# Kernel optimization log

Measured on AMD Instinct MI355X. Metric: run time of the kernel, lower is better.

The kernel has to match this reference:

```python
import jax, jax.numpy as jnp
import numpy as np

N_NODES = 100000
D = 128        # hidden_channels
H = 64         # hidden_size
E = 8192       # num_hyperedges
K = 32         # nodes per hyperedge (fixed group size)


def setup_inputs() -> dict:
    key = jax.random.key(0)
    k1, k2, k3, k4, k5, k6 = jax.random.split(key, 6)
    X = jax.random.normal(k1, (N_NODES, D), dtype=jnp.float32)
    idx = jax.random.randint(k2, (E, K), 0, N_NODES, dtype=jnp.int64)
    # per-hyperedge MLP params (torch Linear: y = x @ W.T + b), scaled like
    # torch's default uniform fan-in init magnitude
    W1 = jax.random.normal(k3, (E, H, D), dtype=jnp.float32) / np.sqrt(D)
    b1 = jax.random.normal(k4, (E, H), dtype=jnp.float32) / np.sqrt(D)
    W2 = jax.random.normal(k5, (E, H), dtype=jnp.float32) / np.sqrt(H)
    b2 = jax.random.normal(k6, (E,), dtype=jnp.float32) / np.sqrt(H)
    return {"X": X, "idx": idx, "W1": W1, "b1": b1, "W2": W2, "b2": b2}


def reference(X, idx, W1, b1, W2, b2):
    # gather node features per hyperedge: [E, K, D]
    x_he = X[idx]
    # per-edge 2-layer MLP scorer (leaky_relu slope 0.01 = torch default)
    h = jax.nn.leaky_relu(jnp.einsum('ekd,ehd->ekh', x_he, W1) + b1[:, None, :])
    w = jnp.einsum('ekh,eh->ek', h, W2) + b2[:, None]          # [E, K]
    beta = jax.nn.softmax(w, axis=1)                           # softmax over group
    z = jnp.einsum('ek,ekd->ed', beta, x_he)                   # weighted sum reduce
    Z = jnp.tanh(jax.nn.leaky_relu(z))                         # [E, D]
    return Z, beta
```

## Files before the change

### kernel.cpp

```cpp
#include <hip/hip_runtime.h>

#define E_EDGES 8192
#define KN 32
#define DD 128
#define HH 64
#define XPAD 8

typedef __attribute__((ext_vector_type(8))) __bf16 bf16x8;
typedef __attribute__((ext_vector_type(8))) unsigned short u16x8;
typedef __attribute__((ext_vector_type(4))) float f32x4;

__device__ __forceinline__ unsigned short f2bf(float f) {
    unsigned int u = __builtin_bit_cast(unsigned int, f);
    u += 0x7FFFu + ((u >> 16) & 1u);
    return (unsigned short)(u >> 16);
}

__device__ __forceinline__ bf16x8 pack_bf8(float4 a, float4 b) {
    u16x8 u;
    u[0] = f2bf(a.x); u[1] = f2bf(a.y); u[2] = f2bf(a.z); u[3] = f2bf(a.w);
    u[4] = f2bf(b.x); u[5] = f2bf(b.y); u[6] = f2bf(b.z); u[7] = f2bf(b.w);
    return __builtin_bit_cast(bf16x8, u);
}

__global__ __launch_bounds__(256, 4)
void he_attn_kernel(const float* __restrict__ X,
                    const int* __restrict__ idx,
                    const float* __restrict__ W1,
                    const float* __restrict__ b1,
                    const float* __restrict__ W2,
                    const float* __restrict__ b2,
                    float* __restrict__ Zout,
                    float* __restrict__ Bout)
{
    const int e    = blockIdx.x;
    const int tid  = threadIdx.x;
    const int lane = tid & 63;
    const int wv   = tid >> 6;
    const int cl   = lane & 15;
    const int kg   = lane >> 4;

    __shared__ unsigned short xsb[KN][DD + XPAD];
    __shared__ float wpart[4][KN];
    __shared__ float beta_s[KN];

    const int j = wv * 16 + cl;
    const float* W1r = W1 + ((size_t)e * HH + j) * DD;
    float4 wf[8];
    #pragma unroll
    for (int kc = 0; kc < 4; ++kc) {
        wf[2 * kc]     = *reinterpret_cast<const float4*>(W1r + kc * 32 + kg * 8);
        wf[2 * kc + 1] = *reinterpret_cast<const float4*>(W1r + kc * 32 + kg * 8 + 4);
    }

    #pragma unroll
    for (int it = 0; it < 4; ++it) {
        int i = tid + it * 256;
        int k = i >> 5;
        int c = i & 31;
        int row = idx[e * KN + k];
        float4 v = reinterpret_cast<const float4*>(X)[(size_t)row * (DD / 4) + c];
        ushort4 bv;
        bv.x = f2bf(v.x); bv.y = f2bf(v.y); bv.z = f2bf(v.z); bv.w = f2bf(v.w);
        *reinterpret_cast<ushort4*>(&xsb[k][c * 4]) = bv;
    }
    __syncthreads();

    f32x4 acc0 = {0.f, 0.f, 0.f, 0.f};
    f32x4 acc1 = {0.f, 0.f, 0.f, 0.f};
    #pragma unroll
    for (int kc = 0; kc < 4; ++kc) {
        const int ds = kc * 32 + kg * 8;
        bf16x8 a0 = *reinterpret_cast<const bf16x8*>(&xsb[cl][ds]);
        bf16x8 a1 = *reinterpret_cast<const bf16x8*>(&xsb[16 + cl][ds]);
        bf16x8 bb = pack_bf8(wf[2 * kc], wf[2 * kc + 1]);
        acc0 = __builtin_amdgcn_mfma_f32_16x16x32_bf16(a0, bb, acc0, 0, 0, 0);
        acc1 = __builtin_amdgcn_mfma_f32_16x16x32_bf16(a1, bb, acc1, 0, 0, 0);
    }

    const float b1j = b1[e * HH + j];
    const float w2j = W2[e * HH + j];
    float pk[8];
    #pragma unroll
    for (int r = 0; r < 4; ++r) {
        float h0 = acc0[r] + b1j; h0 = (h0 > 0.f) ? h0 : 0.01f * h0;
        float h1 = acc1[r] + b1j; h1 = (h1 > 0.f) ? h1 : 0.01f * h1;
        pk[r]     = h0 * w2j;
        pk[4 + r] = h1 * w2j;
    }
    #pragma unroll
    for (int m = 1; m < 16; m <<= 1) {
        #pragma unroll
        for (int q = 0; q < 8; ++q) pk[q] += __shfl_xor(pk[q], m);
    }
    if (cl == 0) {
        #pragma unroll
        for (int r = 0; r < 4; ++r) {
            wpart[wv][kg * 4 + r]      = pk[r];
            wpart[wv][16 + kg * 4 + r] = pk[4 + r];
        }
    }
    __syncthreads();

    if (tid < KN) {
        float v = b2[e] + wpart[0][tid] + wpart[1][tid] + wpart[2][tid] + wpart[3][tid];
        float mx = v;
        #pragma unroll
        for (int off = 16; off >= 1; off >>= 1) mx = fmaxf(mx, __shfl_xor(mx, off));
        float ex = __expf(v - mx);
        float s = ex;
        #pragma unroll
        for (int off = 16; off >= 1; off >>= 1) s += __shfl_xor(s, off);
        float beta = ex / s;
        beta_s[tid] = beta;
        Bout[(size_t)e * KN + tid] = beta;
    }
    __syncthreads();

    if (tid < DD) {
        float z = 0.f;
        #pragma unroll
        for (int k = 0; k < KN; ++k) {
            unsigned int b = xsb[k][tid];
            float xv = __builtin_bit_cast(float, b << 16);
            z += beta_s[k] * xv;
        }
        z = (z > 0.f) ? z : 0.01f * z;
        Zout[(size_t)e * DD + tid] = tanhf(z);
    }
}

extern "C" void kernel_launch(void* const* d_in, const int* in_sizes, int n_in,
                              void* d_out, int out_size, void* d_ws, size_t ws_size,
                              hipStream_t stream) {
    const float* X   = (const float*)d_in[0];
    const int*   idx = (const int*)d_in[1];
    const float* W1  = (const float*)d_in[2];
    const float* b1  = (const float*)d_in[3];
    const float* W2  = (const float*)d_in[4];
    const float* b2  = (const float*)d_in[5];
    float* Zout = (float*)d_out;
    float* Bout = Zout + (size_t)E_EDGES * DD;
    (void)in_sizes; (void)n_in; (void)out_size; (void)d_ws; (void)ws_size;
    he_attn_kernel<<<dim3(E_EDGES), dim3(256), 0, stream>>>(X, idx, W1, b1, W2, b2, Zout, Bout);
}
```

Measured before the change: 64.79 us.

## Process four hyperedges per block with register-prefetched next-edge loads

Each block now handles four consecutive hyperedges in a loop. While one edge is being computed, the X rows and W1 tile for the next edge and the indices for the edge after that are loaded into registers, so global latency overlaps with MFMA and softmax work. Barriers become raw s_barrier calls with explicit lgkmcnt waits, and bf16 conversion uses native casts. The cost is four times fewer blocks (2048) and more registers held for the prefetch buffers, which may lower occupancy.

```diff
diff --git a/kernel.cpp b/kernel.cpp
--- a/kernel.cpp
+++ b/kernel.cpp
@@ -5,22 +5,17 @@
 #define DD 128
 #define HH 64
 #define XPAD 8
+#define EPB 4
+#define NBLK (E_EDGES / EPB)
 
 typedef __attribute__((ext_vector_type(8))) __bf16 bf16x8;
-typedef __attribute__((ext_vector_type(8))) unsigned short u16x8;
+typedef __attribute__((ext_vector_type(4))) __bf16 bf16x4;
 typedef __attribute__((ext_vector_type(4))) float f32x4;
 
-__device__ __forceinline__ unsigned short f2bf(float f) {
-    unsigned int u = __builtin_bit_cast(unsigned int, f);
-    u += 0x7FFFu + ((u >> 16) & 1u);
-    return (unsigned short)(u >> 16);
-}
-
-__device__ __forceinline__ bf16x8 pack_bf8(float4 a, float4 b) {
-    u16x8 u;
-    u[0] = f2bf(a.x); u[1] = f2bf(a.y); u[2] = f2bf(a.z); u[3] = f2bf(a.w);
-    u[4] = f2bf(b.x); u[5] = f2bf(b.y); u[6] = f2bf(b.z); u[7] = f2bf(b.w);
-    return __builtin_bit_cast(bf16x8, u);
+__device__ __forceinline__ void sync_lds() {
+    asm volatile("s_waitcnt lgkmcnt(0)" ::: "memory");
+    __builtin_amdgcn_s_barrier();
+    __builtin_amdgcn_sched_barrier(0);
 }
 
 __global__ __launch_bounds__(256, 4)
@@ -33,100 +28,147 @@
                     float* __restrict__ Zout,
                     float* __restrict__ Bout)
 {
-    const int e    = blockIdx.x;
     const int tid  = threadIdx.x;
     const int lane = tid & 63;
     const int wv   = tid >> 6;
     const int cl   = lane & 15;
     const int kg   = lane >> 4;
+    const int ebase = blockIdx.x * EPB;
+
+    const int r0 = tid >> 5;
+    const int c0 = (tid & 31) * 4;
+    const int j  = wv * 16 + cl;
 
     __shared__ unsigned short xsb[KN][DD + XPAD];
     __shared__ float wpart[4][KN];
     __shared__ float beta_s[KN];
 
-    const int j = wv * 16 + cl;
-    const float* W1r = W1 + ((size_t)e * HH + j) * DD;
+    float b1v[EPB], w2v[EPB], b2v[EPB];
+    #pragma unroll
+    for (int t = 0; t < EPB; ++t) {
+        b1v[t] = b1[(size_t)(ebase + t) * HH + j];
+        w2v[t] = W2[(size_t)(ebase + t) * HH + j];
+        b2v[t] = b2[ebase + t];
+    }
+    int rowc[4];
+    #pragma unroll
+    for (int it = 0; it < 4; ++it) rowc[it] = idx[(size_t)ebase * KN + r0 + 8 * it];
+    float4 xr[4];
+    #pragma unroll
+    for (int it = 0; it < 4; ++it)
+        xr[it] = *reinterpret_cast<const float4*>(X + (size_t)rowc[it] * DD + c0);
     float4 wf[8];
+    {
+        const float* W1r = W1 + ((size_t)ebase * HH + j) * DD;
+        #pragma unroll
+        for (int q = 0; q < 8; ++q)
+            wf[q] = *reinterpret_cast<const float4*>(W1r + (q >> 1) * 32 + kg * 8 + (q & 1) * 4);
+    }
+    int rown[4];
     #pragma unroll
-    for (int kc = 0; kc < 4; ++kc) {
-        wf[2 * kc]     = *reinterpret_cast<const float4*>(W1r + kc * 32 + kg * 8);
-        wf[2 * kc + 1] = *reinterpret_cast<const float4*>(W1r + kc * 32 + kg * 8 + 4);
-    }
+    for (int it = 0; it < 4; ++it)
+        rown[it] = idx[(size_t)(ebase + 1) * KN + r0 + 8 * it];
 
     #pragma unroll
-    for (int it = 0; it < 4; ++it) {
-        int i = tid + it * 256;
-        int k = i >> 5;
-        int c = i & 31;
-        int row = idx[e * KN + k];
-        float4 v = reinterpret_cast<const float4*>(X)[(size_t)row * (DD / 4) + c];
-        ushort4 bv;
-        bv.x = f2bf(v.x); bv.y = f2bf(v.y); bv.z = f2bf(v.z); bv.w = f2bf(v.w);
-        *reinterpret_cast<ushort4*>(&xsb[k][c * 4]) = bv;
-    }
-    __syncthreads();
+    for (int t = 0; t < EPB; ++t) {
+        const int e = ebase + t;
 
-    f32x4 acc0 = {0.f, 0.f, 0.f, 0.f};
-    f32x4 acc1 = {0.f, 0.f, 0.f, 0.f};
-    #pragma unroll
-    for (int kc = 0; kc < 4; ++kc) {
-        const int ds = kc * 32 + kg * 8;
-        bf16x8 a0 = *reinterpret_cast<const bf16x8*>(&xsb[cl][ds]);
-        bf16x8 a1 = *reinterpret_cast<const bf16x8*>(&xsb[16 + cl][ds]);
-        bf16x8 bb = pack_bf8(wf[2 * kc], wf[2 * kc + 1]);
-        acc0 = __builtin_amdgcn_mfma_f32_16x16x32_bf16(a0, bb, acc0, 0, 0, 0);
-        acc1 = __builtin_amdgcn_mfma_f32_16x16x32_bf16(a1, bb, acc1, 0, 0, 0);
-    }
+        bf16x8 bb[4];
+        #pragma unroll
+        for (int kc = 0; kc < 4; ++kc) {
+            float4 a = wf[2 * kc], b = wf[2 * kc + 1];
+            bf16x8 v;
+            v[0] = (__bf16)a.x; v[1] = (__bf16)a.y; v[2] = (__bf16)a.z; v[3] = (__bf16)a.w;
+            v[4] = (__bf16)b.x; v[5] = (__bf16)b.y; v[6] = (__bf16)b.z; v[7] = (__bf16)b.w;
+            bb[kc] = v;
+        }
 
-    const float b1j = b1[e * HH + j];
-    const float w2j = W2[e * HH + j];
-    float pk[8];
-    #pragma unroll
-    for (int r = 0; r < 4; ++r) {
-        float h0 = acc0[r] + b1j; h0 = (h0 > 0.f) ? h0 : 0.01f * h0;
-        float h1 = acc1[r] + b1j; h1 = (h1 > 0.f) ? h1 : 0.01f * h1;
-        pk[r]     = h0 * w2j;
-        pk[4 + r] = h1 * w2j;
-    }
-    #pragma unroll
-    for (int m = 1; m < 16; m <<= 1) {
+        sync_lds();
+
         #pragma unroll
-        for (int q = 0; q < 8; ++q) pk[q] += __shfl_xor(pk[q], m);
-    }
-    if (cl == 0) {
+        for (int it = 0; it < 4; ++it) {
+            bf16x4 bv;
+            bv[0] = (__bf16)xr[it].x; bv[1] = (__bf16)xr[it].y;
+            bv[2] = (__bf16)xr[it].z; bv[3] = (__bf16)xr[it].w;
+            *reinterpret_cast<bf16x4*>(&xsb[r0 + 8 * it][c0]) = bv;
+        }
+
+        if (t + 1 < EPB) {
+            #pragma unroll
+            for (int it = 0; it < 4; ++it)
+                xr[it] = *reinterpret_cast<const float4*>(X + (size_t)rown[it] * DD + c0);
+            const float* W1r = W1 + ((size_t)(e + 1) * HH + j) * DD;
+            #pragma unroll
+            for (int q = 0; q < 8; ++q)
+                wf[q] = *reinterpret_cast<const float4*>(W1r + (q >> 1) * 32 + kg * 8 + (q & 1) * 4);
+        }
+        if (t + 2 < EPB) {
+            #pragma unroll
+            for (int it = 0; it < 4; ++it)
+                rown[it] = idx[(size_t)(e + 2) * KN + r0 + 8 * it];
+        }
+
+        sync_lds();
+
+        f32x4 acc0 = {0.f, 0.f, 0.f, 0.f}, acc1 = {0.f, 0.f, 0.f, 0.f};
+        #pragma unroll
+        for (int kc = 0; kc < 4; ++kc) {
+            const int ds = kc * 32 + kg * 8;
+            bf16x8 a0 = *reinterpret_cast<const bf16x8*>(&xsb[cl][ds]);
+            bf16x8 a1 = *reinterpret_cast<const bf16x8*>(&xsb[16 + cl][ds]);
+            acc0 = __builtin_amdgcn_mfma_f32_16x16x32_bf16(a0, bb[kc], acc0, 0, 0, 0);
+            acc1 = __builtin_amdgcn_mfma_f32_16x16x32_bf16(a1, bb[kc], acc1, 0, 0, 0);
+        }
+
+        float pk[8];
         #pragma unroll
         for (int r = 0; r < 4; ++r) {
-            wpart[wv][kg * 4 + r]      = pk[r];
-            wpart[wv][16 + kg * 4 + r] = pk[4 + r];
+            float h0 = acc0[r] + b1v[t]; h0 = (h0 > 0.f) ? h0 : 0.01f * h0;
+            float h1 = acc1[r] + b1v[t]; h1 = (h1 > 0.f) ? h1 : 0.01f * h1;
+            pk[r]     = h0 * w2v[t];
+            pk[4 + r] = h1 * w2v[t];
         }
-    }
-    __syncthreads();
+        #pragma unroll
+        for (int m = 1; m < 16; m <<= 1) {
+            #pragma unroll
+            for (int q = 0; q < 8; ++q) pk[q] += __shfl_xor(pk[q], m);
+        }
+        if (cl == 0) {
+            #pragma unroll
+            for (int r = 0; r < 4; ++r) {
+                wpart[wv][kg * 4 + r]      = pk[r];
+                wpart[wv][16 + kg * 4 + r] = pk[4 + r];
+            }
+        }
 
-    if (tid < KN) {
-        float v = b2[e] + wpart[0][tid] + wpart[1][tid] + wpart[2][tid] + wpart[3][tid];
-        float mx = v;
-        #pragma unroll
-        for (int off = 16; off >= 1; off >>= 1) mx = fmaxf(mx, __shfl_xor(mx, off));
-        float ex = __expf(v - mx);
-        float s = ex;
-        #pragma unroll
-        for (int off = 16; off >= 1; off >>= 1) s += __shfl_xor(s, off);
-        float beta = ex / s;
-        beta_s[tid] = beta;
-        Bout[(size_t)e * KN + tid] = beta;
-    }
-    __syncthreads();
+        sync_lds();
 
-    if (tid < DD) {
-        float z = 0.f;
-        #pragma unroll
-        for (int k = 0; k < KN; ++k) {
-            unsigned int b = xsb[k][tid];
-            float xv = __builtin_bit_cast(float, b << 16);
-            z += beta_s[k] * xv;
+        if (tid < KN) {
+            float v = b2v[t] + wpart[0][tid] + wpart[1][tid] + wpart[2][tid] + wpart[3][tid];
+            float mx = v;
+            #pragma unroll
+            for (int off = 16; off >= 1; off >>= 1) mx = fmaxf(mx, __shfl_xor(mx, off));
+            float ex = __expf(v - mx);
+            float s = ex;
+            #pragma unroll
+            for (int off = 16; off >= 1; off >>= 1) s += __shfl_xor(s, off);
+            float beta = ex / s;
+            beta_s[tid] = beta;
+            Bout[(size_t)e * KN + tid] = beta;
         }
-        z = (z > 0.f) ? z : 0.01f * z;
-        Zout[(size_t)e * DD + tid] = tanhf(z);
+
+        sync_lds();
+
+        if (tid < DD) {
+            float z = 0.f;
+            #pragma unroll
+            for (int k = 0; k < KN; ++k) {
+                unsigned int bq = xsb[k][tid];
+                z += beta_s[k] * __builtin_bit_cast(float, bq << 16);
+            }
+            z = (z > 0.f) ? z : 0.01f * z;
+            Zout[(size_t)e * DD + tid] = tanhf(z);
+        }
     }
 }
 
@@ -142,5 +184,5 @@
     float* Zout = (float*)d_out;
     float* Bout = Zout + (size_t)E_EDGES * DD;
     (void)in_sizes; (void)n_in; (void)out_size; (void)d_ws; (void)ws_size;
-    he_attn_kernel<<<dim3(E_EDGES), dim3(256), 0, stream>>>(X, idx, W1, b1, W2, b2, Zout, Bout);
+    he_attn_kernel<<<dim3(NBLK), dim3(256), 0, stream>>>(X, idx, W1, b1, W2, b2, Zout, Bout);
 }
```

Measured after the change: 67.14 us. 3.6% more time.
